# Kernel optimization log

Hardware: AMD Instinct MI355X
Metric: run time of the kernel (lower is better)

The kernel has to match this reference:

```python
import jax, jax.numpy as jnp
import numpy as np

B, N, L, D, H, DH = 1, 512, 256, 256, 8, 32  # batch, n_seqs, length, d_msa, heads, d_hidden
EPS = 1e-5


def setup_inputs() -> dict:
    key = jax.random.key(0)
    ks = jax.random.split(key, 3)
    msa = jax.random.normal(ks[0], (B, N, L, D), dtype=jnp.float32)
    # xavier-uniform-ish scale for (H*DH, D) linear weights
    lim = float(np.sqrt(6.0 / (D + H * DH)))
    Wq = jax.random.uniform(ks[1], (H * DH, D), minval=-lim, maxval=lim, dtype=jnp.float32)
    Wk = jax.random.uniform(ks[2], (H * DH, D), minval=-lim, maxval=lim, dtype=jnp.float32)
    return {
        "msa": msa,
        "Wq": Wq,
        "bq": jnp.zeros((H * DH,), jnp.float32),
        "Wk": Wk,
        "bk": jnp.zeros((H * DH,), jnp.float32),
        "ln_gamma": jnp.ones((D,), jnp.float32),
        "ln_beta": jnp.zeros((D,), jnp.float32),
        "stride": 0,
    }


def reference(msa, Wq, bq, Wk, bk, ln_gamma, ln_beta, stride):
    # stride only controls chunking in the original (no math effect); ignored.
    def ln(x):
        m = jnp.mean(x, axis=-1, keepdims=True)
        v = jnp.mean((x - m) ** 2, axis=-1, keepdims=True)
        return (x - m) * jax.lax.rsqrt(v + EPS) * ln_gamma + ln_beta

    scale = 1.0 / np.sqrt(DH)
    b, n, l = msa.shape[:3]
    # query from target (first) sequence: (B, L, H, DH)
    q = (ln(msa[:, 0]) @ Wq.T + bq).reshape(b, l, H, DH) * scale
    # keys from all sequences: (B, N, L, H, DH)
    k = (ln(msa) @ Wk.T + bk).reshape(b, n, l, H, DH)
    # attention logits over the sequence axis N: (B, N, L, H)
    logits = jnp.einsum("blhd,bnlhd->bnlh", q, k)
    attn = jax.nn.softmax(logits, axis=1)
    # dropout is identity in eval mode
    return attn[..., None]  # (B, N, L, H, 1)
```

## Files before the change

kernel.cpp:

```cpp
#include <hip/hip_runtime.h>
#include <hip/hip_bf16.h>
#include <cstdint>

#define LL 256
#define NN 512
#define DD 256
#define HH 8
#define EPSF 1e-5f
#define WGS 264

typedef __attribute__((ext_vector_type(8))) __bf16 bf16x8;
typedef __attribute__((ext_vector_type(4))) float f32x4;

static __device__ __forceinline__ void load_group(
    const float* __restrict__ msa, int l, int wave, int col, int kb, int g,
    float4 (&buf)[16])
{
    const float* rp = msa + ((size_t)(g * 128 + (wave << 4) + col) * LL + l) * DD + (kb << 3);
    #pragma unroll
    for (int ks = 0; ks < 8; ++ks) {
        buf[2 * ks]     = *(const float4*)(rp + ks * 32);
        buf[2 * ks + 1] = *(const float4*)(rp + ks * 32 + 4);
    }
}

static __device__ __forceinline__ void compute_group(
    const float4 (&buf)[16], const bf16x8 (&bfr)[8], f32x4& hacc, f32x4& gacc)
{
    #pragma unroll
    for (int ks = 0; ks < 8; ++ks) {
        float4 u = buf[2 * ks], v = buf[2 * ks + 1];
        bf16x8 a;
        a[0] = (__bf16)u.x; a[1] = (__bf16)u.y; a[2] = (__bf16)u.z; a[3] = (__bf16)u.w;
        a[4] = (__bf16)v.x; a[5] = (__bf16)v.y; a[6] = (__bf16)v.z; a[7] = (__bf16)v.w;
        hacc = __builtin_amdgcn_mfma_f32_16x16x32_bf16(a, bfr[ks], hacc, 0, 0, 0);
        gacc = __builtin_amdgcn_mfma_f32_16x16x32_bf16(a, a,       gacc, 0, 0, 0);
    }
}

static __device__ __forceinline__ void store_group(
    int g, int wave, int col, int kb, const f32x4& hacc, const f32x4& gacc,
    float* logits, float* sS, float* sQ)
{
    const int nb = g * 128 + (wave << 4);
    #pragma unroll
    for (int i = 0; i < 4; ++i) {
        int n = nb + (kb << 2) + i;
        if (col < HH)       logits[col * NN + n] = hacc[i];
        else if (col == HH) sS[n] = hacc[i];
    }
    if (kb == (col >> 2)) sQ[nb + col] = gacc[col & 3];
}

__global__ __launch_bounds__(512, 2) void k_fused(
    const float* __restrict__ msa, const float* __restrict__ Wq,
    const float* __restrict__ bq, const float* __restrict__ Wk,
    const float* __restrict__ gamma, const float* __restrict__ beta,
    float* __restrict__ out)
{
    const int l = blockIdx.x;
    const int tid = threadIdx.x, wave = tid >> 6, lane = tid & 63;
    const int col = lane & 15, kb = lane >> 4;

    __shared__ __align__(16) float logits[HH * NN];
    __shared__ __align__(16) float sS[NN];
    __shared__ __align__(16) float sQ[NN];
    __shared__ __align__(16) __bf16 WgL[16 * WGS];
    __shared__ float lnx[DD];
    __shared__ float qv[DD];
    __shared__ float red[8];
    __shared__ float stats[16];
    __shared__ float Gs[HH];

    {
        float x0 = (tid < DD) ? msa[(size_t)l * DD + tid] : 0.f;
        float s = x0, ss = x0 * x0;
        #pragma unroll
        for (int m = 32; m >= 1; m >>= 1) { s += __shfl_xor(s, m); ss += __shfl_xor(ss, m); }
        if (tid < DD && lane == 0) { red[wave * 2] = s; red[wave * 2 + 1] = ss; }
        __syncthreads();
        if (tid < DD) {
            float sm = red[0] + red[2] + red[4] + red[6];
            float sq = red[1] + red[3] + red[5] + red[7];
            float mean = sm * (1.f / DD);
            float var  = sq * (1.f / DD) - mean * mean;
            float rs   = rsqrtf(var + EPSF);
            lnx[tid] = (x0 - mean) * rs * gamma[tid] + beta[tid];
        }
        __syncthreads();
        const int r = tid & 255, hf = tid >> 8;
        float acc = 0.f;
        {
            const float4* wr = (const float4*)(Wq + (size_t)r * DD) + hf * 32;
            const float* lx = lnx + hf * 128;
            #pragma unroll 4
            for (int j = 0; j < 32; ++j) {
                float4 w4 = wr[j];
                acc += lx[4*j] * w4.x + lx[4*j+1] * w4.y + lx[4*j+2] * w4.z + lx[4*j+3] * w4.w;
            }
        }
        if (hf == 0) qv[r] = acc;
        __syncthreads();
        if (hf == 1) qv[r] = (qv[r] + acc + bq[r]) * 0.17677669529663687f;
        __syncthreads();
        const int c = tid & 255, h0 = (tid >> 8) * 4;
        #pragma unroll
        for (int hi = 0; hi < 4; ++hi) {
            int h = h0 + hi;
            float a = 0.f;
            const float* wk = Wk + ((size_t)h * 32) * DD + c;
            #pragma unroll 8
            for (int d = 0; d < 32; ++d)
                a += qv[h * 32 + d] * wk[(size_t)d * DD];
            WgL[h * WGS + c] = (__bf16)(gamma[c] * a);
        }
        if (tid < DD) {
            WgL[8 * WGS + tid] = (__bf16)1.0f;
        } else {
            const int c2 = tid - 256;
            #pragma unroll
            for (int h = 9; h < 16; ++h) WgL[h * WGS + c2] = (__bf16)0.0f;
        }
        __syncthreads();
        if (wave < HH) {
            float gsum = 0.f;
            #pragma unroll
            for (int i = 0; i < 4; ++i) gsum += (float)WgL[wave * WGS + lane * 4 + i];
            #pragma unroll
            for (int m = 32; m >= 1; m >>= 1) gsum += __shfl_xor(gsum, m);
            if (lane == 0) Gs[wave] = gsum;
        }
        __syncthreads();
    }

    bf16x8 bfr[8];
    #pragma unroll
    for (int ks = 0; ks < 8; ++ks)
        bfr[ks] = *(const bf16x8*)&WgL[col * WGS + ks * 32 + kb * 8];

    float4 A[16], B[16];
    load_group(msa, l, wave, col, kb, 0, A);
    load_group(msa, l, wave, col, kb, 1, B);
    const f32x4 z = {0.f, 0.f, 0.f, 0.f};
    {
        f32x4 ha = z, ga = z;
        compute_group(A, bfr, ha, ga);
        load_group(msa, l, wave, col, kb, 2, A);
        store_group(0, wave, col, kb, ha, ga, logits, sS, sQ);
    }
    {
        f32x4 ha = z, ga = z;
        compute_group(B, bfr, ha, ga);
        load_group(msa, l, wave, col, kb, 3, B);
        store_group(1, wave, col, kb, ha, ga, logits, sS, sQ);
    }
    {
        f32x4 ha = z, ga = z;
        compute_group(A, bfr, ha, ga);
        store_group(2, wave, col, kb, ha, ga, logits, sS, sQ);
    }
    {
        f32x4 ha = z, ga = z;
        compute_group(B, bfr, ha, ga);
        store_group(3, wave, col, kb, ha, ga, logits, sS, sQ);
    }
    __syncthreads();

    {
        const int h = wave;
        const float Gh = Gs[h];
        const float* lp = logits + h * NN;
        float4 ra = ((const float4*)lp)[lane * 2];
        float4 rb = ((const float4*)lp)[lane * 2 + 1];
        float4 sa = ((const float4*)sS)[lane * 2];
        float4 sb = ((const float4*)sS)[lane * 2 + 1];
        float4 qa = ((const float4*)sQ)[lane * 2];
        float4 qb = ((const float4*)sQ)[lane * 2 + 1];
        float raw[8] = {ra.x, ra.y, ra.z, ra.w, rb.x, rb.y, rb.z, rb.w};
        float sv[8]  = {sa.x, sa.y, sa.z, sa.w, sb.x, sb.y, sb.z, sb.w};
        float qv2[8] = {qa.x, qa.y, qa.z, qa.w, qb.x, qb.y, qb.z, qb.w};
        float adj[8];
        #pragma unroll
        for (int i = 0; i < 8; ++i) {
            float mean = sv[i] * (1.f / DD);
            float var  = qv2[i] * (1.f / DD) - mean * mean;
            float rs   = rsqrtf(var + EPSF);
            adj[i] = rs * (raw[i] - mean * Gh);
        }
        float mx = adj[0];
        #pragma unroll
        for (int i = 1; i < 8; ++i) mx = fmaxf(mx, adj[i]);
        #pragma unroll
        for (int m = 32; m >= 1; m >>= 1) mx = fmaxf(mx, __shfl_xor(mx, m));
        float sm = 0.f;
        #pragma unroll
        for (int i = 0; i < 8; ++i) sm += __expf(adj[i] - mx);
        #pragma unroll
        for (int m = 32; m >= 1; m >>= 1) sm += __shfl_xor(sm, m);
        if (lane == 0) { stats[wave] = mx; stats[8 + wave] = 1.f / sm; }
    }
    __syncthreads();

    {
        const int n = tid;
        float s = sS[n], q2 = sQ[n];
        float mean = s * (1.f / DD);
        float var  = q2 * (1.f / DD) - mean * mean;
        float rs   = rsqrtf(var + EPSF);
        float o[8];
        #pragma unroll
        for (int h = 0; h < HH; ++h) {
            float adj = rs * (logits[h * NN + n] - mean * Gs[h]);
            o[h] = __expf(adj - stats[h]) * stats[8 + h];
        }
        float* op = out + (size_t)n * LL * HH + (size_t)l * HH;
        float4 p0 = {o[0], o[1], o[2], o[3]};
        float4 p1 = {o[4], o[5], o[6], o[7]};
        *(float4*)(op)     = p0;
        *(float4*)(op + 4) = p1;
    }
}

extern "C" void kernel_launch(void* const* d_in, const int* in_sizes, int n_in,
                              void* d_out, int out_size, void* d_ws, size_t ws_size,
                              hipStream_t stream) {
    (void)in_sizes; (void)n_in; (void)out_size; (void)d_ws; (void)ws_size;
    const float* msa   = (const float*)d_in[0];
    const float* Wq    = (const float*)d_in[1];
    const float* bq    = (const float*)d_in[2];
    const float* Wk    = (const float*)d_in[3];
    const float* gamma = (const float*)d_in[5];
    const float* beta  = (const float*)d_in[6];
    k_fused<<<dim3(LL), dim3(512), 0, stream>>>(msa, Wq, bq, Wk, gamma, beta, (float*)d_out);
}
```

Before: 43.05 us.

## Stage msa rows through LDS bf16 tile with coalesced row loads and early prefetch

```diff
diff --git a/kernel.cpp b/kernel.cpp
--- a/kernel.cpp
+++ b/kernel.cpp
@@ -8,48 +8,59 @@
 #define HH 8
 #define EPSF 1e-5f
 #define WGS 264
+#define TS  264
 
 typedef __attribute__((ext_vector_type(8))) __bf16 bf16x8;
+typedef __attribute__((ext_vector_type(4))) __bf16 bf16x4;
 typedef __attribute__((ext_vector_type(4))) float f32x4;
 
-static __device__ __forceinline__ void load_group(
-    const float* __restrict__ msa, int l, int wave, int col, int kb, int g,
-    float4 (&buf)[16])
-{
-    const float* rp = msa + ((size_t)(g * 128 + (wave << 4) + col) * LL + l) * DD + (kb << 3);
+static __device__ __forceinline__ void lb_sync() {
+    __builtin_amdgcn_sched_barrier(0);
+    asm volatile("s_waitcnt lgkmcnt(0)" ::: "memory");
+    __builtin_amdgcn_s_barrier();
+    __builtin_amdgcn_sched_barrier(0);
+}
+
+static __device__ __forceinline__ void loadg(
+    const float* __restrict__ msa, int l, int wave, int lane, int t, float4 (&buf)[16])
+{
+    #pragma unroll
+    for (int r = 0; r < 16; ++r)
+        buf[r] = *((const float4*)(msa + ((size_t)(t * 128 + wave * 16 + r) * LL + l) * DD) + lane);
+}
+
+static __device__ __forceinline__ void dswcvt(
+    const float4 (&buf)[16], __bf16* tile, int wave, int lane)
+{
+    #pragma unroll
+    for (int r = 0; r < 16; ++r) {
+        float4 u = buf[r];
+        bf16x4 b;
+        b[0] = (__bf16)u.x; b[1] = (__bf16)u.y; b[2] = (__bf16)u.z; b[3] = (__bf16)u.w;
+        *(bf16x4*)(tile + (wave * 16 + r) * TS + lane * 4) = b;
+    }
+}
+
+static __device__ __forceinline__ void compute_t(
+    int g, const __bf16* tile, const bf16x8 (&bfr)[8], int wave, int col, int kb,
+    float* logits, float* sS, float* sQ)
+{
+    f32x4 ha = {0.f, 0.f, 0.f, 0.f}, ga = {0.f, 0.f, 0.f, 0.f};
+    const __bf16* arow = tile + (wave * 16 + col) * TS;
     #pragma unroll
     for (int ks = 0; ks < 8; ++ks) {
-        buf[2 * ks]     = *(const float4*)(rp + ks * 32);
-        buf[2 * ks + 1] = *(const float4*)(rp + ks * 32 + 4);
-    }
-}
-
-static __device__ __forceinline__ void compute_group(
-    const float4 (&buf)[16], const bf16x8 (&bfr)[8], f32x4& hacc, f32x4& gacc)
-{
-    #pragma unroll
-    for (int ks = 0; ks < 8; ++ks) {
-        float4 u = buf[2 * ks], v = buf[2 * ks + 1];
-        bf16x8 a;
-        a[0] = (__bf16)u.x; a[1] = (__bf16)u.y; a[2] = (__bf16)u.z; a[3] = (__bf16)u.w;
-        a[4] = (__bf16)v.x; a[5] = (__bf16)v.y; a[6] = (__bf16)v.z; a[7] = (__bf16)v.w;
-        hacc = __builtin_amdgcn_mfma_f32_16x16x32_bf16(a, bfr[ks], hacc, 0, 0, 0);
-        gacc = __builtin_amdgcn_mfma_f32_16x16x32_bf16(a, a,       gacc, 0, 0, 0);
-    }
-}
-
-static __device__ __forceinline__ void store_group(
-    int g, int wave, int col, int kb, const f32x4& hacc, const f32x4& gacc,
-    float* logits, float* sS, float* sQ)
-{
-    const int nb = g * 128 + (wave << 4);
+        bf16x8 a = *(const bf16x8*)(arow + ks * 32 + kb * 8);
+        ha = __builtin_amdgcn_mfma_f32_16x16x32_bf16(a, bfr[ks], ha, 0, 0, 0);
+        ga = __builtin_amdgcn_mfma_f32_16x16x32_bf16(a, a,       ga, 0, 0, 0);
+    }
+    const int nb = g * 128 + wave * 16;
     #pragma unroll
     for (int i = 0; i < 4; ++i) {
         int n = nb + (kb << 2) + i;
-        if (col < HH)       logits[col * NN + n] = hacc[i];
-        else if (col == HH) sS[n] = hacc[i];
-    }
-    if (kb == (col >> 2)) sQ[nb + col] = gacc[col & 3];
+        if (col < HH)       logits[col * NN + n] = ha[i];
+        else if (col == HH) sS[n] = ha[i];
+    }
+    if (kb == (col >> 2)) sQ[nb + col] = ga[col & 3];
 }
 
 __global__ __launch_bounds__(512, 2) void k_fused(
@@ -62,23 +73,28 @@
     const int tid = threadIdx.x, wave = tid >> 6, lane = tid & 63;
     const int col = lane & 15, kb = lane >> 4;
 
+    __shared__ __align__(16) __bf16 tile[128 * TS];
+    __shared__ __align__(16) __bf16 WgL[16 * WGS];
     __shared__ __align__(16) float logits[HH * NN];
     __shared__ __align__(16) float sS[NN];
     __shared__ __align__(16) float sQ[NN];
-    __shared__ __align__(16) __bf16 WgL[16 * WGS];
     __shared__ float lnx[DD];
     __shared__ float qv[DD];
     __shared__ float red[8];
     __shared__ float stats[16];
     __shared__ float Gs[HH];
 
+    float4 P[16], Q[16];
+    loadg(msa, l, wave, lane, 0, P);
+    loadg(msa, l, wave, lane, 1, Q);
+
     {
         float x0 = (tid < DD) ? msa[(size_t)l * DD + tid] : 0.f;
         float s = x0, ss = x0 * x0;
         #pragma unroll
         for (int m = 32; m >= 1; m >>= 1) { s += __shfl_xor(s, m); ss += __shfl_xor(ss, m); }
         if (tid < DD && lane == 0) { red[wave * 2] = s; red[wave * 2 + 1] = ss; }
-        __syncthreads();
+        lb_sync();
         if (tid < DD) {
             float sm = red[0] + red[2] + red[4] + red[6];
             float sq = red[1] + red[3] + red[5] + red[7];
@@ -87,7 +103,7 @@
             float rs   = rsqrtf(var + EPSF);
             lnx[tid] = (x0 - mean) * rs * gamma[tid] + beta[tid];
         }
-        __syncthreads();
+        lb_sync();
         const int r = tid & 255, hf = tid >> 8;
         float acc = 0.f;
         {
@@ -100,10 +116,11 @@
             }
         }
         if (hf == 0) qv[r] = acc;
-        __syncthreads();
+        lb_sync();
         if (hf == 1) qv[r] = (qv[r] + acc + bq[r]) * 0.17677669529663687f;
-        __syncthreads();
+        lb_sync();
         const int c = tid & 255, h0 = (tid >> 8) * 4;
+        const float gm = gamma[c];
         #pragma unroll
         for (int hi = 0; hi < 4; ++hi) {
             int h = h0 + hi;
@@ -112,7 +129,7 @@
             #pragma unroll 8
             for (int d = 0; d < 32; ++d)
                 a += qv[h * 32 + d] * wk[(size_t)d * DD];
-            WgL[h * WGS + c] = (__bf16)(gamma[c] * a);
+            WgL[h * WGS + c] = (__bf16)(gm * a);
         }
         if (tid < DD) {
             WgL[8 * WGS + tid] = (__bf16)1.0f;
@@ -121,7 +138,7 @@
             #pragma unroll
             for (int h = 9; h < 16; ++h) WgL[h * WGS + c2] = (__bf16)0.0f;
         }
-        __syncthreads();
+        lb_sync();
         if (wave < HH) {
             float gsum = 0.f;
             #pragma unroll
@@ -130,7 +147,7 @@
             for (int m = 32; m >= 1; m >>= 1) gsum += __shfl_xor(gsum, m);
             if (lane == 0) Gs[wave] = gsum;
         }
-        __syncthreads();
+        lb_sync();
     }
 
     bf16x8 bfr[8];
@@ -138,33 +155,14 @@
     for (int ks = 0; ks < 8; ++ks)
         bfr[ks] = *(const bf16x8*)&WgL[col * WGS + ks * 32 + kb * 8];
 
-    float4 A[16], B[16];
-    load_group(msa, l, wave, col, kb, 0, A);
-    load_group(msa, l, wave, col, kb, 1, B);
-    const f32x4 z = {0.f, 0.f, 0.f, 0.f};
-    {
-        f32x4 ha = z, ga = z;
-        compute_group(A, bfr, ha, ga);
-        load_group(msa, l, wave, col, kb, 2, A);
-        store_group(0, wave, col, kb, ha, ga, logits, sS, sQ);
-    }
-    {
-        f32x4 ha = z, ga = z;
-        compute_group(B, bfr, ha, ga);
-        load_group(msa, l, wave, col, kb, 3, B);
-        store_group(1, wave, col, kb, ha, ga, logits, sS, sQ);
-    }
-    {
-        f32x4 ha = z, ga = z;
-        compute_group(A, bfr, ha, ga);
-        store_group(2, wave, col, kb, ha, ga, logits, sS, sQ);
-    }
-    {
-        f32x4 ha = z, ga = z;
-        compute_group(B, bfr, ha, ga);
-        store_group(3, wave, col, kb, ha, ga, logits, sS, sQ);
-    }
-    __syncthreads();
+    dswcvt(P, tile, wave, lane);  loadg(msa, l, wave, lane, 2, P);  lb_sync();
+    compute_t(0, tile, bfr, wave, col, kb, logits, sS, sQ);         lb_sync();
+    dswcvt(Q, tile, wave, lane);  loadg(msa, l, wave, lane, 3, Q);  lb_sync();
+    compute_t(1, tile, bfr, wave, col, kb, logits, sS, sQ);         lb_sync();
+    dswcvt(P, tile, wave, lane);                                    lb_sync();
+    compute_t(2, tile, bfr, wave, col, kb, logits, sS, sQ);         lb_sync();
+    dswcvt(Q, tile, wave, lane);                                    lb_sync();
+    compute_t(3, tile, bfr, wave, col, kb, logits, sS, sQ);         lb_sync();
 
     {
         const int h = wave;
@@ -199,7 +197,7 @@
         for (int m = 32; m >= 1; m >>= 1) sm += __shfl_xor(sm, m);
         if (lane == 0) { stats[wave] = mx; stats[8 + wave] = 1.f / sm; }
     }
-    __syncthreads();
+    lb_sync();
 
     {
         const int n = tid;
```

New measurement: 44.77 us. +4.0%, slower.
